# Kernel tuning notes

Hardware: AMD Instinct MI355X
Metric: run time of the kernel (lower is better)

Reference implementation:

```python
import jax, jax.numpy as jnp
import numpy as np

S = 2048        # seq_len (number of rigid bodies)
D = 256         # node_dim
H = 16          # num_heads
C = 64          # num_channels
SPATIAL_DIM = 3
QUATERNION_DIM = 4


def setup_inputs() -> dict:
    key = jax.random.key(0)
    ks = jax.random.split(key, 9)
    nodes = jax.random.normal(ks[0], (S, D), jnp.float32)
    pos = jax.random.normal(ks[1], (S, 2 * SPATIAL_DIM), jnp.float32)
    rot = jax.random.normal(ks[2], (S, QUATERNION_DIM), jnp.float32)
    w = 0.02
    Wn = jax.random.normal(ks[3], (2 * H * C, D), jnp.float32) * w
    bn = jnp.zeros((2 * H * C,), jnp.float32)
    Wp = jax.random.normal(ks[4], (2 * H * C, 2 * SPATIAL_DIM), jnp.float32) * w
    bp = jnp.zeros((2 * H * C,), jnp.float32)
    Wr = jax.random.normal(ks[5], (2 * H * C, QUATERNION_DIM), jnp.float32) * w  # no bias
    Wv = jax.random.normal(ks[6], (3 * H * D, D), jnp.float32) * w
    bv = jnp.zeros((3 * H * D,), jnp.float32)
    return {"nodes": nodes, "pos": pos, "rot": rot,
            "Wn": Wn, "bn": bn, "Wp": Wp, "bp": bp, "Wr": Wr,
            "Wv": Wv, "bv": bv}


def _kq(x, W, b):
    # eqx.nn.Linear: y = W @ x + b, vmapped over seq -> x @ W.T + b
    y = x @ W.T
    if b is not None:
        y = y + b
    y = y.reshape(x.shape[0], H, 2 * C)
    k, q = jnp.split(y, 2, axis=-1)  # each (S, H, C)
    return k, q


def reference(nodes, pos, rot, Wn, bn, Wp, bp, Wr, Wv, bv):
    seq_len = nodes.shape[0]
    nodes_k, nodes_q = _kq(nodes, Wn, bn)
    pos_k, pos_q = _kq(pos, Wp, bp)
    rot_k, rot_q = _kq(rot, Wr, None)
    k = jnp.concatenate([nodes_k, pos_k, rot_k], axis=-2)  # (S, 3H, C)
    q = jnp.concatenate([nodes_q, pos_q, rot_q], axis=-2)  # (S, 3H, C)
    val = (nodes @ Wv.T + bv).reshape(seq_len, 3 * H, D)   # (S, 3H, D)
    logits = jnp.einsum('ihc,jhc->ijh', k, q)              # (S, S, 3H)
    # square the rotation-source logits (last H of the 3H head axis)
    logits = logits.at[..., -H:].set(jnp.square(logits[..., -H:]))
    logits = logits / jnp.sqrt(jnp.float32(H))
    att = jax.nn.softmax(logits, axis=-2)                  # softmax over key axis j
    out = jnp.einsum('ijh,jhd->id', att, val)              # (S, D)
    return out
```

## Files before the change

### kernel.cpp

```cpp
#include <hip/hip_runtime.h>
#include <hip/hip_bf16.h>

typedef __bf16 bf16;
typedef __attribute__((ext_vector_type(8)))  __bf16 bf16x8;
typedef __attribute__((ext_vector_type(4)))  __bf16 bf16x4;
typedef __attribute__((ext_vector_type(4)))  float  f32x4;

#define SEQ   2048
#define NDIM  256
#define NH3   48
#define CH    64
#define SQS   72
#define SVS   72
#define SPS   72
#define VTS   2176

#define OFF_NODES 0
#define OFF_POS   524288
#define OFF_ROT   536576
#define OFF_WN    544768
#define OFF_BN    1069056
#define OFF_WP    1071104
#define OFF_BP    1083392
#define OFF_WR    1085440
#define OFF_WV    1093632
#define OFF_BV    4239360
#define TOT_IN    4251648

__device__ bf16  g_in[TOT_IN];
__device__ bf16  g_k [NH3 * SEQ * CH];
__device__ bf16  g_q [NH3 * SEQ * CH];
__device__ bf16  g_vt[NH3 * NDIM * VTS];
__device__ float g_part[(size_t)NH3 * SEQ * NDIM];
__device__ int   g_isf32;

__global__ __launch_bounds__(256) void detect_k(const unsigned short* __restrict__ p) {
    __shared__ int cff, czero;
    if (threadIdx.x == 0) { cff = 0; czero = 0; }
    __syncthreads();
    int ff = 0, zz = 0;
    for (int r = 0; r < 64; ++r) {
        int idx = threadIdx.x * 64 + r;
        unsigned short u = p[idx];
        if (((u >> 7) & 0xFF) == 0xFF) ff++;
        if (((idx & 1) == 0) && (u == 0)) zz++;
    }
    if (ff) atomicAdd(&cff, ff);
    if (zz) atomicAdd(&czero, zz);
    __syncthreads();
    if (threadIdx.x == 0) g_isf32 = (cff > 2 || czero > 6000) ? 1 : 0;
}

__global__ __launch_bounds__(256) void convert_k(
    const void* s0, const void* s1, const void* s2, const void* s3, const void* s4,
    const void* s5, const void* s6, const void* s7, const void* s8, const void* s9)
{
    const void* srcs[10] = {s0, s1, s2, s3, s4, s5, s6, s7, s8, s9};
    const int   szs[10]  = {524288, 12288, 8192, 524288, 2048, 12288, 2048, 8192, 3145728, 12288};
    const int   offs[10] = {OFF_NODES, OFF_POS, OFF_ROT, OFF_WN, OFF_BN,
                            OFF_WP, OFF_BP, OFF_WR, OFF_WV, OFF_BV};
    const int y = blockIdx.y;
    const void* src = srcs[y];
    bf16* dst = g_in + offs[y];
    const int n = szs[y];
    const int isf = g_isf32;
    const int stride = gridDim.x * 256 * 4;
    for (int i = (blockIdx.x * 256 + threadIdx.x) * 4; i < n; i += stride) {
        bf16x4 o;
        if (isf) {
            float4 v = *(const float4*)((const float*)src + i);
            o[0] = (bf16)v.x; o[1] = (bf16)v.y; o[2] = (bf16)v.z; o[3] = (bf16)v.w;
        } else {
            o = *(const bf16x4*)((const bf16*)src + i);
        }
        *(bf16x4*)(dst + i) = o;
    }
}

__global__ __launch_bounds__(256) void proj_all()
{
    __shared__ __align__(16) bf16 sB[64 * 264];
    __shared__ __align__(16) bf16 sO[64 * 72];
    const int t  = threadIdx.x;
    const int gb = blockIdx.x;

    if (gb < 1024) {
        const bf16* nodes = g_in + OFF_NODES;
        const bf16* Wn    = g_in + OFF_WN;
        const bf16* bn    = g_in + OFF_BN;
        const int bx   = gb;
        const int xcd  = bx & 7;
        const int rest = bx >> 3;
        const int f0   = (xcd * 4 + (rest & 3)) * 64;
        const int s0   = (rest >> 2) * 64;

        for (int rep = 0; rep < 8; ++rep) {
            int idx = t + rep * 256;
            int row = idx >> 5, chunk = idx & 31;
            *(bf16x8*)&sB[row * 264 + chunk * 8] =
                *(const bf16x8*)&Wn[(f0 + row) * 256 + chunk * 8];
        }
        __syncthreads();

        const int w = t >> 6, lane = t & 63;
        const int l15 = lane & 15, quad = lane >> 4;

        f32x4 acc[4] = {{}, {}, {}, {}};
        const bf16* arow = nodes + (s0 + w * 16 + l15) * 256 + quad * 8;
#pragma unroll
        for (int kc = 0; kc < 8; ++kc) {
            bf16x8 af = *(const bf16x8*)(arow + kc * 32);
#pragma unroll
            for (int ft = 0; ft < 4; ++ft) {
                bf16x8 bfr = *(const bf16x8*)&sB[(ft * 16 + l15) * 264 + kc * 32 + quad * 8];
                acc[ft] = __builtin_amdgcn_mfma_f32_16x16x32_bf16(af, bfr, acc[ft], 0, 0, 0);
            }
        }
#pragma unroll
        for (int ft = 0; ft < 4; ++ft) {
            int f = f0 + ft * 16 + l15;
            float bias = (float)bn[f];
            int h = f >> 7, c2 = f & 127;
            bf16* base = (c2 < 64) ? (g_k + h * SEQ * CH + c2)
                                   : (g_q + h * SEQ * CH + (c2 - 64));
#pragma unroll
            for (int r = 0; r < 4; ++r) {
                int s = s0 + w * 16 + quad * 4 + r;
                base[s * CH] = (bf16)(acc[ft][r] + bias);
            }
        }
    } else if (gb < 9216) {
        const bf16* pos  = g_in + OFF_POS;
        const bf16* rotq = g_in + OFF_ROT;
        const bf16* Wp   = g_in + OFF_WP;
        const bf16* bp   = g_in + OFF_BP;
        const bf16* Wr   = g_in + OFF_WR;
        int id = (gb - 1024) * 256 + t;
        int fg  = id & 511;
        int s   = (id >> 9) & 2047;
        int src = id >> 20;
        int f0  = fg * 4;
        float y[4]; int h;
        if (src == 0) {
#pragma unroll
            for (int j = 0; j < 4; ++j) {
                float a = (float)bp[f0 + j];
#pragma unroll
                for (int x = 0; x < 6; ++x)
                    a += (float)pos[s * 6 + x] * (float)Wp[(f0 + j) * 6 + x];
                y[j] = a;
            }
            h = 16 + (f0 >> 7);
        } else {
#pragma unroll
            for (int j = 0; j < 4; ++j) {
                float a = 0.f;
#pragma unroll
                for (int x = 0; x < 4; ++x)
                    a += (float)rotq[s * 4 + x] * (float)Wr[(f0 + j) * 4 + x];
                y[j] = a;
            }
            h = 32 + (f0 >> 7);
        }
        bf16x4 o;
#pragma unroll
        for (int j = 0; j < 4; ++j) o[j] = (bf16)y[j];
        int c2 = f0 & 127;
        if (c2 < 64) *(bf16x4*)&g_k[(h * SEQ + s) * CH + c2]        = o;
        else         *(bf16x4*)&g_q[(h * SEQ + s) * CH + (c2 - 64)] = o;
    } else {
        const bf16* nodes = g_in + OFF_NODES;
        const bf16* Wv    = g_in + OFF_WV;
        const bf16* bv    = g_in + OFF_BV;
        const int bx   = gb - 9216;
        const int xcd  = bx & 7;
        const int rest = bx >> 3;
        const int f0   = (xcd * 24 + (rest % 24)) * 64;
        const int s0   = (rest / 24) * 64;

        for (int rep = 0; rep < 8; ++rep) {
            int idx = t + rep * 256;
            int row = idx >> 5, chunk = idx & 31;
            *(bf16x8*)&sB[row * 264 + chunk * 8] =
                *(const bf16x8*)&Wv[(size_t)(f0 + row) * 256 + chunk * 8];
        }
        __syncthreads();

        const int w = t >> 6, lane = t & 63;
        const int l15 = lane & 15, quad = lane >> 4;

        f32x4 acc[4] = {{}, {}, {}, {}};
        const bf16* arow = nodes + (s0 + w * 16 + l15) * 256 + quad * 8;
#pragma unroll
        for (int kc = 0; kc < 8; ++kc) {
            bf16x8 af = *(const bf16x8*)(arow + kc * 32);
#pragma unroll
            for (int ft = 0; ft < 4; ++ft) {
                bf16x8 bfr = *(const bf16x8*)&sB[(ft * 16 + l15) * 264 + kc * 32 + quad * 8];
                acc[ft] = __builtin_amdgcn_mfma_f32_16x16x32_bf16(af, bfr, acc[ft], 0, 0, 0);
            }
        }
        __syncthreads();
#pragma unroll
        for (int ft = 0; ft < 4; ++ft) {
            int n = f0 + ft * 16 + l15;
            float bias = (float)bv[n];
#pragma unroll
            for (int r = 0; r < 4; ++r) {
                sO[(ft * 16 + l15) * 72 + (quad * 4 + r) * 4 + w] = (bf16)(acc[ft][r] + bias);
            }
        }
        __syncthreads();
        for (int rep = 0; rep < 2; ++rep) {
            int idx = t + rep * 256;
            int row = idx >> 3, chunk = idx & 7;
            *(bf16x8*)&g_vt[(size_t)(f0 + row) * VTS + s0 + chunk * 8] =
                *(const bf16x8*)&sO[row * 72 + chunk * 8];
        }
    }
}

__global__ __launch_bounds__(512, 4) void attn_k()
{
    const int bx  = blockIdx.x;
    const int xcd = bx & 7;
    const int sub = bx >> 3;
    const int h   = xcd * 6 + (sub % 6);
    const int it  = sub / 6;
    const int i0  = it * 128;
    const int t   = threadIdx.x;
    const int w   = t >> 6, lane = t & 63;
    const int l15 = lane & 15, quad = lane >> 4;
    const bool rot = (h >= 32);

    __shared__ __align__(16) bf16 sQ[64 * SQS];
    __shared__ __align__(16) bf16 sV[256 * SVS];
    __shared__ __align__(16) bf16 sP[128 * SPS];
    __shared__ float sL[128];

    const bf16* kb = g_k  + h * SEQ * CH;
    const bf16* qb = g_q  + h * SEQ * CH;
    const bf16* vb = g_vt + (size_t)h * NDIM * VTS;

    bf16x8 kf0 = *(const bf16x8*)&kb[(i0 + w * 16 + l15) * CH + quad * 8];
    bf16x8 kf1 = *(const bf16x8*)&kb[(i0 + w * 16 + l15) * CH + 32 + quad * 8];

    const int ih = w >> 2, dq = w & 3;

    const int qrow = t >> 3, qch = t & 7;

    f32x4 acc[4][4];
#pragma unroll
    for (int a = 0; a < 4; ++a)
#pragma unroll
        for (int b = 0; b < 4; ++b) acc[a][b] = (f32x4){0.f, 0.f, 0.f, 0.f};
    f32x4 lp = {0.f, 0.f, 0.f, 0.f};

    bf16x8 qpre, vpre[4];
    qpre = *(const bf16x8*)&qb[t * 8];
#pragma unroll
    for (int rep = 0; rep < 4; ++rep) {
        int idx = t + rep * 512;
        vpre[rep] = *(const bf16x8*)&vb[(size_t)(idx >> 3) * VTS + (idx & 7) * 8];
    }
    *(bf16x8*)&sQ[qrow * SQS + qch * 8] = qpre;
#pragma unroll
    for (int rep = 0; rep < 4; ++rep) {
        int idx = t + rep * 512;
        *(bf16x8*)&sV[(idx >> 3) * SVS + (idx & 7) * 8] = vpre[rep];
    }
    __syncthreads();

    for (int st = 0; st < 32; ++st) {
        f32x4 sjb[4];
#pragma unroll
        for (int jb = 0; jb < 4; ++jb) {
            bf16x8 q0 = *(const bf16x8*)&sQ[(jb * 16 + l15) * SQS + quad * 8];
            bf16x8 q1 = *(const bf16x8*)&sQ[(jb * 16 + l15) * SQS + 32 + quad * 8];
            f32x4 sa = {};
            sa = __builtin_amdgcn_mfma_f32_16x16x32_bf16(kf0, q0, sa, 0, 0, 0);
            sa = __builtin_amdgcn_mfma_f32_16x16x32_bf16(kf1, q1, sa, 0, 0, 0);
            sjb[jb] = sa;
        }

#pragma unroll
        for (int r = 0; r < 4; ++r) {
            bf16x4 pk;
#pragma unroll
            for (int jb = 0; jb < 4; ++jb) {
                float d = sjb[jb][r];
                float x = rot ? (d * d * 0.25f) : (d * 0.25f);
                x = fminf(x, 60.f);
                float p = __expf(x);
                lp[r] += p;
                pk[jb] = (bf16)p;
            }
            *(bf16x4*)&sP[(w * 16 + quad * 4 + r) * SPS + l15 * 4] = pk;
        }
        __syncthreads();

        if (st < 31) {
            const bf16* qn = qb + (st + 1) * 4096;
            const bf16* vn = vb + (st + 1) * 64;
            qpre = *(const bf16x8*)&qn[t * 8];
#pragma unroll
            for (int rep = 0; rep < 4; ++rep) {
                int idx = t + rep * 512;
                vpre[rep] = *(const bf16x8*)&vn[(size_t)(idx >> 3) * VTS + (idx & 7) * 8];
            }
        }

#pragma unroll
        for (int kc = 0; kc < 2; ++kc) {
            bf16x8 ap[4], vf[4];
#pragma unroll
            for (int itr = 0; itr < 4; ++itr)
                ap[itr] = *(const bf16x8*)&sP[(ih * 64 + itr * 16 + l15) * SPS + kc * 32 + quad * 8];
#pragma unroll
            for (int dt = 0; dt < 4; ++dt)
                vf[dt] = *(const bf16x8*)&sV[(dq * 64 + dt * 16 + l15) * SVS + kc * 32 + quad * 8];
#pragma unroll
            for (int itr = 0; itr < 4; ++itr)
#pragma unroll
                for (int dt = 0; dt < 4; ++dt)
                    acc[itr][dt] = __builtin_amdgcn_mfma_f32_16x16x32_bf16(
                        ap[itr], vf[dt], acc[itr][dt], 0, 0, 0);
        }
        __syncthreads();

        if (st < 31) {
            *(bf16x8*)&sQ[qrow * SQS + qch * 8] = qpre;
#pragma unroll
            for (int rep = 0; rep < 4; ++rep) {
                int idx = t + rep * 512;
                *(bf16x8*)&sV[(idx >> 3) * SVS + (idx & 7) * 8] = vpre[rep];
            }
            __syncthreads();
        }
    }

#pragma unroll
    for (int off = 1; off < 16; off <<= 1) {
#pragma unroll
        for (int r = 0; r < 4; ++r) lp[r] += __shfl_xor(lp[r], off, 64);
    }
    if (l15 == 0) *(f32x4*)&sL[w * 16 + quad * 4] = lp;
    __syncthreads();

    float* pb = g_part + (size_t)h * SEQ * NDIM;
#pragma unroll
    for (int itr = 0; itr < 4; ++itr) {
        f32x4 lv = *(const f32x4*)&sL[ih * 64 + itr * 16 + quad * 4];
#pragma unroll
        for (int r = 0; r < 4; ++r) {
            float inv = 1.0f / lv[r];
            float* ob = &pb[(size_t)(i0 + ih * 64 + itr * 16 + quad * 4 + r) * NDIM + dq * 64 + l15];
#pragma unroll
            for (int dt = 0; dt < 4; ++dt)
                ob[dt * 16] = acc[itr][dt][r] * inv;
        }
    }
}

__global__ __launch_bounds__(256) void finalize_k(float* __restrict__ out) {
    int idx = (blockIdx.x * 256 + threadIdx.x) * 4;
    f32x4 s = {0.f, 0.f, 0.f, 0.f};
#pragma unroll
    for (int hh = 0; hh < NH3; ++hh)
        s += *(const f32x4*)&g_part[(size_t)hh * SEQ * NDIM + idx];
    *(f32x4*)&out[idx] = s;
}

extern "C" void kernel_launch(void* const* d_in, const int* in_sizes, int n_in,
                              void* d_out, int out_size, void* d_ws, size_t ws_size,
                              hipStream_t stream) {
    detect_k <<<dim3(1),        dim3(256), 0, stream>>>((const unsigned short*)d_in[8]);
    convert_k<<<dim3(768, 10),  dim3(256), 0, stream>>>(d_in[0], d_in[1], d_in[2], d_in[3],
                                                        d_in[4], d_in[5], d_in[6], d_in[7],
                                                        d_in[8], d_in[9]);
    proj_all  <<<dim3(15360),   dim3(256), 0, stream>>>();
    attn_k    <<<dim3(768),     dim3(512), 0, stream>>>();
    finalize_k<<<dim3(512),     dim3(256), 0, stream>>>((float*)d_out);
}
```

Measured before the change: 331.0 us.

## Split attention key range in two blocks per tile, combine with normalization

```diff
diff --git a/kernel.cpp b/kernel.cpp
--- a/kernel.cpp
+++ b/kernel.cpp
@@ -31,7 +31,9 @@
 __device__ bf16  g_k [NH3 * SEQ * CH];
 __device__ bf16  g_q [NH3 * SEQ * CH];
 __device__ bf16  g_vt[NH3 * NDIM * VTS];
-__device__ float g_part[(size_t)NH3 * SEQ * NDIM];
+__device__ float g_part[(size_t)2 * NH3 * SEQ * NDIM];
+__device__ float g_l   [2 * NH3 * SEQ];
+__device__ float g_invl[NH3 * SEQ];
 __device__ int   g_isf32;
 
 __global__ __launch_bounds__(256) void detect_k(const unsigned short* __restrict__ p) {
@@ -226,7 +228,9 @@
     const int xcd = bx & 7;
     const int sub = bx >> 3;
     const int h   = xcd * 6 + (sub % 6);
-    const int it  = sub / 6;
+    const int rest = sub / 6;
+    const int it  = rest & 15;
+    const int jh  = rest >> 4;
     const int i0  = it * 128;
     const int t   = threadIdx.x;
     const int w   = t >> 6, lane = t & 63;
@@ -236,11 +240,11 @@
     __shared__ __align__(16) bf16 sQ[64 * SQS];
     __shared__ __align__(16) bf16 sV[256 * SVS];
     __shared__ __align__(16) bf16 sP[128 * SPS];
-    __shared__ float sL[128];
 
     const bf16* kb = g_k  + h * SEQ * CH;
-    const bf16* qb = g_q  + h * SEQ * CH;
+    const bf16* qb = g_q  + h * SEQ * CH + jh * 16 * 4096;
     const bf16* vb = g_vt + (size_t)h * NDIM * VTS;
+    const int   jcol0 = jh * 16 * 64;
 
     bf16x8 kf0 = *(const bf16x8*)&kb[(i0 + w * 16 + l15) * CH + quad * 8];
     bf16x8 kf1 = *(const bf16x8*)&kb[(i0 + w * 16 + l15) * CH + 32 + quad * 8];
@@ -261,7 +265,7 @@
 #pragma unroll
     for (int rep = 0; rep < 4; ++rep) {
         int idx = t + rep * 512;
-        vpre[rep] = *(const bf16x8*)&vb[(size_t)(idx >> 3) * VTS + (idx & 7) * 8];
+        vpre[rep] = *(const bf16x8*)&vb[(size_t)(idx >> 3) * VTS + jcol0 + (idx & 7) * 8];
     }
     *(bf16x8*)&sQ[qrow * SQS + qch * 8] = qpre;
 #pragma unroll
@@ -271,7 +275,7 @@
     }
     __syncthreads();
 
-    for (int st = 0; st < 32; ++st) {
+    for (int st = 0; st < 16; ++st) {
         f32x4 sjb[4];
 #pragma unroll
         for (int jb = 0; jb < 4; ++jb) {
@@ -299,9 +303,9 @@
         }
         __syncthreads();
 
-        if (st < 31) {
+        if (st < 15) {
             const bf16* qn = qb + (st + 1) * 4096;
-            const bf16* vn = vb + (st + 1) * 64;
+            const bf16* vn = vb + jcol0 + (st + 1) * 64;
             qpre = *(const bf16x8*)&qn[t * 8];
 #pragma unroll
             for (int rep = 0; rep < 4; ++rep) {
@@ -328,7 +332,7 @@
         }
         __syncthreads();
 
-        if (st < 31) {
+        if (st < 15) {
             *(bf16x8*)&sQ[qrow * SQS + qch * 8] = qpre;
 #pragma unroll
             for (int rep = 0; rep < 4; ++rep) {
@@ -344,30 +348,44 @@
 #pragma unroll
         for (int r = 0; r < 4; ++r) lp[r] += __shfl_xor(lp[r], off, 64);
     }
-    if (l15 == 0) *(f32x4*)&sL[w * 16 + quad * 4] = lp;
-    __syncthreads();
-
-    float* pb = g_part + (size_t)h * SEQ * NDIM;
+    if (l15 == 0)
+        *(f32x4*)&g_l[(jh * NH3 + h) * SEQ + i0 + w * 16 + quad * 4] = lp;
+
+    float* pb = g_part + (size_t)(jh * NH3 + h) * SEQ * NDIM;
 #pragma unroll
     for (int itr = 0; itr < 4; ++itr) {
-        f32x4 lv = *(const f32x4*)&sL[ih * 64 + itr * 16 + quad * 4];
 #pragma unroll
         for (int r = 0; r < 4; ++r) {
-            float inv = 1.0f / lv[r];
             float* ob = &pb[(size_t)(i0 + ih * 64 + itr * 16 + quad * 4 + r) * NDIM + dq * 64 + l15];
 #pragma unroll
             for (int dt = 0; dt < 4; ++dt)
-                ob[dt * 16] = acc[itr][dt][r] * inv;
-        }
-    }
+                ob[dt * 16] = acc[itr][dt][r];
+        }
+    }
+}
+
+__global__ __launch_bounds__(256) void invl_k() {
+    int idx = (blockIdx.x * 256 + threadIdx.x) * 4;
+    f32x4 a = *(const f32x4*)&g_l[idx];
+    f32x4 b = *(const f32x4*)&g_l[NH3 * SEQ + idx];
+    f32x4 o;
+#pragma unroll
+    for (int j = 0; j < 4; ++j) o[j] = 1.0f / (a[j] + b[j]);
+    *(f32x4*)&g_invl[idx] = o;
 }
 
 __global__ __launch_bounds__(256) void finalize_k(float* __restrict__ out) {
     int idx = (blockIdx.x * 256 + threadIdx.x) * 4;
+    int i = idx >> 8;
     f32x4 s = {0.f, 0.f, 0.f, 0.f};
 #pragma unroll
-    for (int hh = 0; hh < NH3; ++hh)
-        s += *(const f32x4*)&g_part[(size_t)hh * SEQ * NDIM + idx];
+    for (int hh = 0; hh < NH3; ++hh) {
+        f32x4 a = *(const f32x4*)&g_part[(size_t)hh * SEQ * NDIM + idx];
+        f32x4 b = *(const f32x4*)&g_part[(size_t)(NH3 + hh) * SEQ * NDIM + idx];
+        float wv = g_invl[hh * SEQ + i];
+#pragma unroll
+        for (int j = 0; j < 4; ++j) s[j] += (a[j] + b[j]) * wv;
+    }
     *(f32x4*)&out[idx] = s;
 }
 
@@ -379,6 +397,7 @@
                                                         d_in[4], d_in[5], d_in[6], d_in[7],
                                                         d_in[8], d_in[9]);
     proj_all  <<<dim3(15360),   dim3(256), 0, stream>>>();
-    attn_k    <<<dim3(768),     dim3(512), 0, stream>>>();
+    attn_k    <<<dim3(1536),    dim3(512), 0, stream>>>();
+    invl_k    <<<dim3(96),      dim3(256), 0, stream>>>();
     finalize_k<<<dim3(512),     dim3(256), 0, stream>>>((float*)d_out);
 }
```

After: 356.6 us. 7.7% more time.
